# Performance work log

Hardware: AMD Instinct MI355X
Metric: run time of the kernel (lower is better)

Reference implementation:

```python
import jax, jax.numpy as jnp
import numpy as np

N_NODES = 200000
N_EDGES = 500000
F_IN = 165
HIDDEN = 384
OUT = 2


def setup_inputs() -> dict:
    key = jax.random.key(0)
    ks = jax.random.split(key, 8)
    x = jax.random.normal(ks[0], (N_NODES, F_IN), dtype=jnp.float32)
    edge_index = jax.random.randint(ks[1], (2, N_EDGES), 0, N_NODES, dtype=jnp.int64)
    # Glorot-ish init for GCNConv weights, zero bias (PyG default)
    def glorot(k, fan_in, fan_out):
        lim = (6.0 / (fan_in + fan_out)) ** 0.5
        return jax.random.uniform(k, (fan_in, fan_out), dtype=jnp.float32, minval=-lim, maxval=lim)
    W1 = glorot(ks[2], F_IN, HIDDEN)
    b1 = jnp.zeros((HIDDEN,), dtype=jnp.float32)
    W2 = glorot(ks[3], HIDDEN, HIDDEN)
    b2 = jnp.zeros((HIDDEN,), dtype=jnp.float32)
    W3 = glorot(ks[4], HIDDEN, OUT)
    b3 = jnp.zeros((OUT,), dtype=jnp.float32)
    return {"x": x, "edge_index": edge_index,
            "W1": W1, "b1": b1, "W2": W2, "b2": b2, "W3": W3, "b3": b3}


def _gcn_norm(edge_index, num_nodes):
    # PyG gcn_norm: add self-loops, symmetric normalization D^-1/2 (A+I) D^-1/2
    loop = jnp.arange(num_nodes, dtype=edge_index.dtype)
    row = jnp.concatenate([edge_index[0], loop])
    col = jnp.concatenate([edge_index[1], loop])
    ones = jnp.ones(row.shape[0], dtype=jnp.float32)
    deg = jax.ops.segment_sum(ones, col, num_segments=num_nodes)
    dinv = jnp.where(deg > 0, jax.lax.rsqrt(deg), 0.0)
    norm = dinv[row] * dinv[col]  # [E + N]
    return row, col, norm


def _gcn_conv(h, W, b, row, col, norm, num_nodes):
    h = h @ W                          # [N, F_out] linear transform first
    msg = h[row] * norm[:, None]       # gather + scale, [E+N, F_out]
    agg = jax.ops.segment_sum(msg, col, num_segments=num_nodes)
    return agg + b


def reference(x, edge_index, W1, b1, W2, b2, W3, b3):
    n = x.shape[0]
    row, col, norm = _gcn_norm(edge_index, n)
    h = jax.nn.relu(_gcn_conv(x, W1, b1, row, col, norm, n))
    h = jax.nn.relu(_gcn_conv(h, W2, b2, row, col, norm, n))
    return _gcn_conv(h, W3, b3, row, col, norm, n)
```

## Files before the change

kernel.cpp:

```cpp
#include <hip/hip_runtime.h>
#include <hip/hip_bf16.h>

#define N_NODES 200000
#define N_EDGES 500000
#define F_IN    165
#define HIDDEN  384
#define F_OUT   2

#define KPAD1   192
#define M_TILES 1563
#define M_PAD   (M_TILES * 128)
#define NB_SCAN 782
#define GRID_GEMM (196 * 24)

typedef unsigned short ushort_t;
typedef unsigned int   uint_t;

using bf16x8 = __attribute__((ext_vector_type(8))) short;
using f32x4  = __attribute__((ext_vector_type(4))) float;

__device__ __forceinline__ float bf2f(uint_t u) {
    return __uint_as_float(u << 16);
}
__device__ __forceinline__ ushort_t f2bf(float x) {
    uint_t b = __float_as_uint(x);
    return (ushort_t)((b + 0x7FFFu + ((b >> 16) & 1u)) >> 16);
}

__global__ void count_kernel(const int* __restrict__ col, int* __restrict__ cnt, int E) {
    int e = blockIdx.x * blockDim.x + threadIdx.x;
    if (e < E) atomicAdd(&cnt[col[e]], 1);
}

__global__ void dinv_kernel(const int* __restrict__ cnt, float* __restrict__ dinv, int n) {
    int i = blockIdx.x * blockDim.x + threadIdx.x;
    if (i < n) dinv[i] = rsqrtf((float)(cnt[i] + 1));
}

__global__ __launch_bounds__(256) void scan1_kernel(const int* __restrict__ cnt,
                                                    int* __restrict__ loc,
                                                    int* __restrict__ bsum, int N) {
    __shared__ int sh[256];
    int t = threadIdx.x;
    int i = blockIdx.x * 256 + t;
    int v = (i < N) ? cnt[i] : 0;
    sh[t] = v;
    __syncthreads();
    #pragma unroll
    for (int off = 1; off < 256; off <<= 1) {
        int u = (t >= off) ? sh[t - off] : 0;
        __syncthreads();
        sh[t] += u;
        __syncthreads();
    }
    int incl = sh[t];
    if (i < N) loc[i] = incl - v;
    if (t == 255) bsum[blockIdx.x] = incl;
}

__global__ __launch_bounds__(1024) void scan2_kernel(int* __restrict__ bsum, int NB) {
    __shared__ int sh[1024];
    int t = threadIdx.x;
    int v = (t < NB) ? bsum[t] : 0;
    sh[t] = v;
    __syncthreads();
    #pragma unroll
    for (int off = 1; off < 1024; off <<= 1) {
        int u = (t >= off) ? sh[t - off] : 0;
        __syncthreads();
        sh[t] += u;
        __syncthreads();
    }
    if (t < NB) bsum[t] = sh[t] - v;
}

__global__ __launch_bounds__(256) void scan3_kernel(int* __restrict__ ptr,
                                                    int* __restrict__ cursor,
                                                    const int* __restrict__ bsum,
                                                    int N, int E) {
    int t = threadIdx.x;
    int i = blockIdx.x * 256 + t;
    if (i < N) {
        int p = ptr[i] + bsum[blockIdx.x];
        ptr[i] = p;
        cursor[i] = p;
    }
    if (i == 0) ptr[N] = E;
}

__global__ void scatter_kernel(const int* __restrict__ row, const int* __restrict__ col,
                               const float* __restrict__ dinv,
                               int* __restrict__ cursor,
                               int* __restrict__ row_srt, float* __restrict__ nrm_srt, int E) {
    int e = blockIdx.x * blockDim.x + threadIdx.x;
    if (e >= E) return;
    int r = row[e], c = col[e];
    int pos = atomicAdd(&cursor[c], 1);
    row_srt[pos] = r;
    nrm_srt[pos] = dinv[r] * dinv[c];
}

__global__ void convx_kernel(const float* __restrict__ X, uint_t* __restrict__ Xb, int total) {
    int idx = blockIdx.x * blockDim.x + threadIdx.x;
    if (idx >= total) return;
    int node = idx / 96, ui = idx - node * 96;
    int f = ui * 2;
    const float* xr = X + (size_t)node * F_IN;
    float lo = (f < F_IN) ? xr[f] : 0.0f;
    float hi = (f + 1 < F_IN) ? xr[f + 1] : 0.0f;
    Xb[idx] = (uint_t)f2bf(lo) | ((uint_t)f2bf(hi) << 16);
}

__global__ __launch_bounds__(256) void agg165b_kernel(
        const uint_t* __restrict__ Xb, const float* __restrict__ dinv,
        const int* __restrict__ ptr, const int* __restrict__ row_srt,
        const float* __restrict__ nrm_srt, ushort_t* __restrict__ out, int N) {
    int w    = (blockIdx.x * blockDim.x + threadIdx.x) >> 6;
    int lane = threadIdx.x & 63;
    if (w >= N) return;
    float d2 = dinv[w]; d2 *= d2;
    const uint_t* self = Xb + (size_t)w * 96;
    bool two = (lane < 19);
    uint_t u0 = self[lane];
    uint_t u1 = two ? self[64 + lane] : 0u;
    float ax0 = bf2f(u0 & 0xFFFFu) * d2, ay0 = bf2f(u0 >> 16) * d2;
    float ax1 = bf2f(u1 & 0xFFFFu) * d2, ay1 = bf2f(u1 >> 16) * d2;
    int e0 = ptr[w], e1 = ptr[w + 1];
    for (int e = e0; e < e1; ++e) {
        int r = row_srt[e];
        float wg = nrm_srt[e];
        const uint_t* hr = Xb + (size_t)r * 96;
        uint_t v0 = hr[lane];
        uint_t v1 = two ? hr[64 + lane] : 0u;
        ax0 = fmaf(bf2f(v0 & 0xFFFFu), wg, ax0);
        ay0 = fmaf(bf2f(v0 >> 16), wg, ay0);
        ax1 = fmaf(bf2f(v1 & 0xFFFFu), wg, ax1);
        ay1 = fmaf(bf2f(v1 >> 16), wg, ay1);
    }
    uint_t* o = (uint_t*)(out + (size_t)w * KPAD1);
    o[lane] = (uint_t)f2bf(ax0) | ((uint_t)f2bf(ay0) << 16);
    if (two) o[64 + lane] = (uint_t)f2bf(ax1) | ((uint_t)f2bf(ay1) << 16);
}

__global__ __launch_bounds__(256) void agg384_kernel(
        const ushort_t* __restrict__ H, const float* __restrict__ dinv,
        const int* __restrict__ ptr, const int* __restrict__ row_srt,
        const float* __restrict__ nrm_srt, ushort_t* __restrict__ out, int N) {
    int w    = (blockIdx.x * blockDim.x + threadIdx.x) >> 6;
    int lane = threadIdx.x & 63;
    if (w >= N) return;
    float d2 = dinv[w]; d2 *= d2;
    const uint_t* self = (const uint_t*)(H + (size_t)w * HIDDEN);
    float ax[3], ay[3];
    #pragma unroll
    for (int j = 0; j < 3; ++j) {
        uint_t u = self[lane + 64 * j];
        ax[j] = bf2f(u & 0xFFFFu) * d2;
        ay[j] = bf2f(u >> 16) * d2;
    }
    int e0 = ptr[w], e1 = ptr[w + 1];
    for (int e = e0; e < e1; ++e) {
        int r = row_srt[e];
        float wg = nrm_srt[e];
        const uint_t* hr = (const uint_t*)(H + (size_t)r * HIDDEN);
        #pragma unroll
        for (int j = 0; j < 3; ++j) {
            uint_t u = hr[lane + 64 * j];
            ax[j] = fmaf(bf2f(u & 0xFFFFu), wg, ax[j]);
            ay[j] = fmaf(bf2f(u >> 16), wg, ay[j]);
        }
    }
    uint_t* o = (uint_t*)(out + (size_t)w * HIDDEN);
    #pragma unroll
    for (int j = 0; j < 3; ++j)
        o[lane + 64 * j] = (uint_t)f2bf(ax[j]) | ((uint_t)f2bf(ay[j]) << 16);
}

__global__ void prep_wt_kernel(const float* __restrict__ W, ushort_t* __restrict__ Wt,
                               int Kin, int Kpad, int Nn) {
    int idx = blockIdx.x * blockDim.x + threadIdx.x;
    if (idx >= Nn * Kpad) return;
    int n = idx / Kpad, k = idx - n * Kpad;
    float v = (k < Kin) ? W[(size_t)k * Nn + n] : 0.0f;
    Wt[idx] = f2bf(v);
}

#define GBK 32

template<bool RELU>
__global__ __launch_bounds__(256) void mfma_gemm_kernel(
        const ushort_t* __restrict__ A, const ushort_t* __restrict__ Wt,
        const float* __restrict__ bias, ushort_t* __restrict__ C,
        int Ks, int Nn, int nTilesM) {
    __shared__ ushort_t As[128 * GBK];
    __shared__ ushort_t Bs[128 * GBK];

    const int l  = blockIdx.x;
    const int g  = l / 24;
    const int r_ = l - g * 24;
    const int cb = r_ >> 3;
    const int pm = r_ & 7;
    const int pt = g * 8 + pm;
    if (pt >= nTilesM) return;
    const int bm = pt * 128;
    const int bn = cb * 128;

    const int tid  = threadIdx.x;
    const int lane = tid & 63;
    const int w    = tid >> 6;
    const int wm   = w & 1;
    const int wn   = w >> 1;

    const int rA = tid >> 2;
    const int q  = tid & 3;

    auto lds_off = [](int row, int chunk) {
        return row * GBK + ((chunk ^ ((row >> 1) & 3)) * 8);
    };
    const int wOff0 = lds_off(rA, q);
    const int wOff1 = lds_off(rA + 64, q);

    auto brow = [](int s) {
        return ((s >> 6) * 64) + ((s & 63) >> 4) + ((s & 15) * 4);
    };
    const int gB0 = brow(rA);
    const int gB1 = brow(rA + 64);

    const ushort_t* Ag0 = A  + (size_t)(bm + rA) * Ks + q * 8;
    const ushort_t* Ag1 = Ag0 + (size_t)64 * Ks;
    const ushort_t* Bg0 = Wt + (size_t)(bn + gB0) * Ks + q * 8;
    const ushort_t* Bg1 = Wt + (size_t)(bn + gB1) * Ks + q * 8;

    const int p     = lane & 15;
    const int khalf = lane >> 4;
    const int qf    = khalf ^ ((p >> 1) & 3);
    int aoff[4], boff[4];
    #pragma unroll
    for (int f = 0; f < 4; ++f) {
        aoff[f] = (wm * 64 + f * 16 + p) * GBK + qf * 8;
        boff[f] = (wn * 64 + f * 16 + p) * GBK + qf * 8;
    }

    f32x4 acc[4][4] = {};

    const int ksteps = Ks >> 5;
    uint4 va0 = *reinterpret_cast<const uint4*>(Ag0);
    uint4 va1 = *reinterpret_cast<const uint4*>(Ag1);
    uint4 vb0 = *reinterpret_cast<const uint4*>(Bg0);
    uint4 vb1 = *reinterpret_cast<const uint4*>(Bg1);

    for (int kt = 0; kt < ksteps; ++kt) {
        __syncthreads();
        *reinterpret_cast<uint4*>(&As[wOff0]) = va0;
        *reinterpret_cast<uint4*>(&As[wOff1]) = va1;
        *reinterpret_cast<uint4*>(&Bs[wOff0]) = vb0;
        *reinterpret_cast<uint4*>(&Bs[wOff1]) = vb1;
        __syncthreads();

        if (kt + 1 < ksteps) {
            const int k0 = (kt + 1) * GBK;
            va0 = *reinterpret_cast<const uint4*>(Ag0 + k0);
            va1 = *reinterpret_cast<const uint4*>(Ag1 + k0);
            vb0 = *reinterpret_cast<const uint4*>(Bg0 + k0);
            vb1 = *reinterpret_cast<const uint4*>(Bg1 + k0);
        }

        bf16x8 af[4], bfr[4];
        #pragma unroll
        for (int f = 0; f < 4; ++f) {
            af[f]  = *reinterpret_cast<const bf16x8*>(&As[aoff[f]]);
            bfr[f] = *reinterpret_cast<const bf16x8*>(&Bs[boff[f]]);
        }
        #pragma unroll
        for (int mi = 0; mi < 4; ++mi)
            #pragma unroll
            for (int ni = 0; ni < 4; ++ni)
                acc[mi][ni] = __builtin_amdgcn_mfma_f32_16x16x32_bf16(
                    af[mi], bfr[ni], acc[mi][ni], 0, 0, 0);
    }

    const int colbase = bn + wn * 64 + p * 4;
    const float4 bb = *reinterpret_cast<const float4*>(bias + colbase);
    const float bias4[4] = {bb.x, bb.y, bb.z, bb.w};
    #pragma unroll
    for (int mi = 0; mi < 4; ++mi) {
        const int rowbase = bm + wm * 64 + mi * 16 + khalf * 4;
        #pragma unroll
        for (int j = 0; j < 4; ++j) {
            float v0 = acc[mi][0][j] + bias4[0];
            float v1 = acc[mi][1][j] + bias4[1];
            float v2 = acc[mi][2][j] + bias4[2];
            float v3 = acc[mi][3][j] + bias4[3];
            if (RELU) {
                v0 = fmaxf(v0, 0.f); v1 = fmaxf(v1, 0.f);
                v2 = fmaxf(v2, 0.f); v3 = fmaxf(v3, 0.f);
            }
            ushort4 o;
            o.x = f2bf(v0); o.y = f2bf(v1); o.z = f2bf(v2); o.w = f2bf(v3);
            *reinterpret_cast<ushort4*>(C + (size_t)(rowbase + j) * Nn + colbase) = o;
        }
    }
}

__global__ __launch_bounds__(256) void gemm_n2_kernel(
        const ushort_t* __restrict__ A, const float* __restrict__ W,
        float* __restrict__ G, int M) {
    int w    = (blockIdx.x * blockDim.x + threadIdx.x) >> 6;
    int lane = threadIdx.x & 63;
    if (w >= M) return;
    const uint_t* a = (const uint_t*)(A + (size_t)w * HIDDEN);
    float s0 = 0.f, s1 = 0.f;
    #pragma unroll
    for (int j = 0; j < 3; ++j) {
        int f2 = lane + 64 * j;
        uint_t u = a[f2];
        float alo = bf2f(u & 0xFFFFu), ahi = bf2f(u >> 16);
        int k = f2 * 2;
        s0 = fmaf(alo, W[k * 2 + 0], s0);
        s1 = fmaf(alo, W[k * 2 + 1], s1);
        s0 = fmaf(ahi, W[k * 2 + 2], s0);
        s1 = fmaf(ahi, W[k * 2 + 3], s1);
    }
    #pragma unroll
    for (int off = 32; off; off >>= 1) {
        s0 += __shfl_down(s0, off);
        s1 += __shfl_down(s1, off);
    }
    if (lane == 0) { G[(size_t)w * 2] = s0; G[(size_t)w * 2 + 1] = s1; }
}

__global__ void out_kernel(const float* __restrict__ G, const float* __restrict__ dinv,
                           const int* __restrict__ ptr, const int* __restrict__ row_srt,
                           const float* __restrict__ nrm_srt, const float* __restrict__ b3,
                           float* __restrict__ out, int N) {
    int i = blockIdx.x * blockDim.x + threadIdx.x;
    if (i >= N) return;
    float d2 = dinv[i]; d2 *= d2;
    float a0 = G[(size_t)i * 2 + 0] * d2 + b3[0];
    float a1 = G[(size_t)i * 2 + 1] * d2 + b3[1];
    int e0 = ptr[i], e1 = ptr[i + 1];
    for (int e = e0; e < e1; ++e) {
        int r = row_srt[e];
        float wg = nrm_srt[e];
        a0 = fmaf(G[(size_t)r * 2 + 0], wg, a0);
        a1 = fmaf(G[(size_t)r * 2 + 1], wg, a1);
    }
    out[(size_t)i * 2 + 0] = a0;
    out[(size_t)i * 2 + 1] = a1;
}

extern "C" void kernel_launch(void* const* d_in, const int* in_sizes, int n_in,
                              void* d_out, int out_size, void* d_ws, size_t ws_size,
                              hipStream_t stream) {
    const float* x   = (const float*)d_in[0];
    const int*   ei  = (const int*)  d_in[1];
    const float* W1  = (const float*)d_in[2];
    const float* b1  = (const float*)d_in[3];
    const float* W2  = (const float*)d_in[4];
    const float* b2  = (const float*)d_in[5];
    const float* W3  = (const float*)d_in[6];
    const float* b3  = (const float*)d_in[7];
    float* out = (float*)d_out;

    const int N = N_NODES, E = N_EDGES;
    const int* row = ei;
    const int* col = ei + E;

    size_t off = 0;
    auto alloc = [&](size_t bytes) { size_t o = off; off += (bytes + 255) & ~(size_t)255; return o; };
    size_t o_dinv   = alloc((size_t)N * 4);
    size_t o_ptr    = alloc((size_t)(N + 1) * 4);
    size_t o_cnt    = alloc((size_t)N * 4);
    size_t o_cursor = alloc((size_t)N * 4);
    size_t o_bsum   = alloc((size_t)NB_SCAN * 4);
    size_t o_rowsrt = alloc((size_t)E * 4);
    size_t o_nrmsrt = alloc((size_t)E * 4);
    size_t o_G      = alloc((size_t)N * 2 * 4);
    size_t o_Wt1    = alloc((size_t)HIDDEN * KPAD1 * 2);
    size_t o_Wt2    = alloc((size_t)HIDDEN * HIDDEN * 2);
    size_t o_B1     = alloc((size_t)M_PAD * HIDDEN * 2);
    size_t o_B2     = alloc((size_t)M_PAD * HIDDEN * 2);
    if (ws_size < off) return;

    char* ws = (char*)d_ws;
    float*    dinv    = (float*)(ws + o_dinv);
    int*      ptr     = (int*)  (ws + o_ptr);
    int*      cnt     = (int*)  (ws + o_cnt);
    int*      cursor  = (int*)  (ws + o_cursor);
    int*      bsum    = (int*)  (ws + o_bsum);
    int*      row_srt = (int*)  (ws + o_rowsrt);
    float*    nrm_srt = (float*)(ws + o_nrmsrt);
    float*    G       = (float*)(ws + o_G);
    ushort_t* Wt1     = (ushort_t*)(ws + o_Wt1);
    ushort_t* Wt2     = (ushort_t*)(ws + o_Wt2);
    ushort_t* B1      = (ushort_t*)(ws + o_B1);
    ushort_t* B2      = (ushort_t*)(ws + o_B2);
    uint_t*   Xb      = (uint_t*)B2;

    const int B = 256;

    prep_wt_kernel<<<(HIDDEN * KPAD1 + B - 1) / B, B, 0, stream>>>(W1, Wt1, F_IN, KPAD1, HIDDEN);
    prep_wt_kernel<<<(HIDDEN * HIDDEN + B - 1) / B, B, 0, stream>>>(W2, Wt2, HIDDEN, HIDDEN, HIDDEN);
    convx_kernel<<<(N * 96 + B - 1) / B, B, 0, stream>>>(x, Xb, N * 96);

    hipMemsetAsync(cnt, 0, (size_t)N * 4, stream);
    count_kernel<<<(E + B - 1) / B, B, 0, stream>>>(col, cnt, E);
    dinv_kernel<<<(N + B - 1) / B, B, 0, stream>>>(cnt, dinv, N);
    scan1_kernel<<<NB_SCAN, 256, 0, stream>>>(cnt, ptr, bsum, N);
    scan2_kernel<<<1, 1024, 0, stream>>>(bsum, NB_SCAN);
    scan3_kernel<<<NB_SCAN, 256, 0, stream>>>(ptr, cursor, bsum, N, E);
    scatter_kernel<<<(E + B - 1) / B, B, 0, stream>>>(row, col, dinv, cursor, row_srt, nrm_srt, E);

    agg165b_kernel<<<(N * 64 + B - 1) / B, B, 0, stream>>>(Xb, dinv, ptr, row_srt, nrm_srt, B1, N);

    mfma_gemm_kernel<true><<<GRID_GEMM, 256, 0, stream>>>(B1, Wt1, b1, B2, KPAD1, HIDDEN, M_TILES);

    agg384_kernel<<<(N * 64 + B - 1) / B, B, 0, stream>>>(B2, dinv, ptr, row_srt, nrm_srt, B1, N);

    mfma_gemm_kernel<true><<<GRID_GEMM, 256, 0, stream>>>(B1, Wt2, b2, B2, HIDDEN, HIDDEN, M_TILES);

    gemm_n2_kernel<<<(N * 64 + B - 1) / B, B, 0, stream>>>(B2, W3, G, N);

    out_kernel<<<(N + B - 1) / B, B, 0, stream>>>(G, dinv, ptr, row_srt, nrm_srt, b3, out, N);
}
```

Baseline: 508.4 us.

## Double-buffer GEMM tiles with direct global-to-LDS async loads

The bf16 MFMA GEMM now loads its A and B tiles straight into LDS with global_load_lds instead of staging them through registers. LDS is double-buffered, so there is one barrier per k-step and the next tile's loads overlap the current tile's MFMAs. Global addresses are permuted so the XOR swizzle in LDS still matches the fragment reads. This doubles LDS use per block and depends on the barrier waiting for the async loads to finish, which is a correctness risk.

```diff
diff --git a/kernel.cpp b/kernel.cpp
--- a/kernel.cpp
+++ b/kernel.cpp
@@ -25,6 +25,13 @@
 __device__ __forceinline__ ushort_t f2bf(float x) {
     uint_t b = __float_as_uint(x);
     return (ushort_t)((b + 0x7FFFu + ((b >> 16) & 1u)) >> 16);
+}
+
+__device__ __forceinline__ void async16(const ushort_t* g, ushort_t* l) {
+    __builtin_amdgcn_global_load_lds(
+        (const __attribute__((address_space(1))) void*)g,
+        (__attribute__((address_space(3))) void*)l,
+        16, 0, 0);
 }
 
 __global__ void count_kernel(const int* __restrict__ col, int* __restrict__ cnt, int E) {
@@ -192,8 +199,8 @@
         const ushort_t* __restrict__ A, const ushort_t* __restrict__ Wt,
         const float* __restrict__ bias, ushort_t* __restrict__ C,
         int Ks, int Nn, int nTilesM) {
-    __shared__ ushort_t As[128 * GBK];
-    __shared__ ushort_t Bs[128 * GBK];
+    __shared__ ushort_t As[2][128 * GBK];
+    __shared__ ushort_t Bs[2][128 * GBK];
 
     const int l  = blockIdx.x;
     const int g  = l / 24;
@@ -211,25 +218,20 @@
     const int wm   = w & 1;
     const int wn   = w >> 1;
 
-    const int rA = tid >> 2;
-    const int q  = tid & 3;
-
-    auto lds_off = [](int row, int chunk) {
-        return row * GBK + ((chunk ^ ((row >> 1) & 3)) * 8);
-    };
-    const int wOff0 = lds_off(rA, q);
-    const int wOff1 = lds_off(rA + 64, q);
-
     auto brow = [](int s) {
         return ((s >> 6) * 64) + ((s & 63) >> 4) + ((s & 15) * 4);
     };
-    const int gB0 = brow(rA);
-    const int gB1 = brow(rA + 64);
-
-    const ushort_t* Ag0 = A  + (size_t)(bm + rA) * Ks + q * 8;
-    const ushort_t* Ag1 = Ag0 + (size_t)64 * Ks;
-    const ushort_t* Bg0 = Wt + (size_t)(bn + gB0) * Ks + q * 8;
-    const ushort_t* Bg1 = Wt + (size_t)(bn + gB1) * Ks + q * 8;
+
+    const int r0  = w * 32;
+    const int s0  = r0 + (lane >> 2);
+    const int s1  = s0 + 16;
+    const int c0  = (lane & 3) ^ ((s0 >> 1) & 3);
+    const int c1  = (lane & 3) ^ ((s1 >> 1) & 3);
+
+    const ushort_t* gA0 = A + (size_t)(bm + s0) * Ks + c0 * 8;
+    const ushort_t* gA1 = A + (size_t)(bm + s1) * Ks + c1 * 8;
+    const ushort_t* gB0 = Wt + (size_t)(bn + brow(s0)) * Ks + c0 * 8;
+    const ushort_t* gB1 = Wt + (size_t)(bn + brow(s1)) * Ks + c1 * 8;
 
     const int p     = lane & 15;
     const int khalf = lane >> 4;
@@ -244,32 +246,31 @@
     f32x4 acc[4][4] = {};
 
     const int ksteps = Ks >> 5;
-    uint4 va0 = *reinterpret_cast<const uint4*>(Ag0);
-    uint4 va1 = *reinterpret_cast<const uint4*>(Ag1);
-    uint4 vb0 = *reinterpret_cast<const uint4*>(Bg0);
-    uint4 vb1 = *reinterpret_cast<const uint4*>(Bg1);
-
+    {
+        async16(gA0, &As[0][r0 * GBK]);
+        async16(gA1, &As[0][(r0 + 16) * GBK]);
+        async16(gB0, &Bs[0][r0 * GBK]);
+        async16(gB1, &Bs[0][(r0 + 16) * GBK]);
+    }
+
+    int cur = 0;
     for (int kt = 0; kt < ksteps; ++kt) {
         __syncthreads();
-        *reinterpret_cast<uint4*>(&As[wOff0]) = va0;
-        *reinterpret_cast<uint4*>(&As[wOff1]) = va1;
-        *reinterpret_cast<uint4*>(&Bs[wOff0]) = vb0;
-        *reinterpret_cast<uint4*>(&Bs[wOff1]) = vb1;
-        __syncthreads();
 
         if (kt + 1 < ksteps) {
-            const int k0 = (kt + 1) * GBK;
-            va0 = *reinterpret_cast<const uint4*>(Ag0 + k0);
-            va1 = *reinterpret_cast<const uint4*>(Ag1 + k0);
-            vb0 = *reinterpret_cast<const uint4*>(Bg0 + k0);
-            vb1 = *reinterpret_cast<const uint4*>(Bg1 + k0);
+            const int ko = (kt + 1) * GBK;
+            const int nb = cur ^ 1;
+            async16(gA0 + ko, &As[nb][r0 * GBK]);
+            async16(gA1 + ko, &As[nb][(r0 + 16) * GBK]);
+            async16(gB0 + ko, &Bs[nb][r0 * GBK]);
+            async16(gB1 + ko, &Bs[nb][(r0 + 16) * GBK]);
         }
 
         bf16x8 af[4], bfr[4];
         #pragma unroll
         for (int f = 0; f < 4; ++f) {
-            af[f]  = *reinterpret_cast<const bf16x8*>(&As[aoff[f]]);
-            bfr[f] = *reinterpret_cast<const bf16x8*>(&Bs[boff[f]]);
+            af[f]  = *reinterpret_cast<const bf16x8*>(&As[cur][aoff[f]]);
+            bfr[f] = *reinterpret_cast<const bf16x8*>(&Bs[cur][boff[f]]);
         }
         #pragma unroll
         for (int mi = 0; mi < 4; ++mi)
@@ -277,6 +278,7 @@
             for (int ni = 0; ni < 4; ++ni)
                 acc[mi][ni] = __builtin_amdgcn_mfma_f32_16x16x32_bf16(
                     af[mi], bfr[ni], acc[mi][ni], 0, 0, 0);
+        cur ^= 1;
     }
 
     const int colbase = bn + wn * 64 + p * 4;
```

Measured after the change: 510.6 us. Within noise of the previous version (+0.4%).
